# Kernel optimization log

Measured on AMD Instinct MI355X. Metric: run time of the kernel, lower is better.

Reference implementation:

```python
import jax, jax.numpy as jnp
import numpy as np

N, E, D = 50000, 800000, 256

def setup_inputs() -> dict:
    key = jax.random.key(0)
    ks = jax.random.split(key, 12)
    s = 1.0 / np.sqrt(D)
    return {
        "x": jax.random.normal(ks[0], (N, D), dtype=jnp.float32),
        "src": jax.random.randint(ks[1], (E,), 0, N, dtype=jnp.int64),
        "dst": jax.random.randint(ks[2], (E,), 0, N, dtype=jnp.int64),
        "W_w": jax.random.normal(ks[3], (D, D), dtype=jnp.float32) * s,
        "W_b": jnp.zeros((D,), dtype=jnp.float32),
        "U_w": jax.random.normal(ks[4], (D, D), dtype=jnp.float32) * s,
        "U_b": jnp.zeros((D,), dtype=jnp.float32),
        "V_w": jax.random.normal(ks[5], (D, D), dtype=jnp.float32) * s,
        "V_b": jnp.zeros((D,), dtype=jnp.float32),
        "attn_l": jax.random.normal(ks[6], (D,), dtype=jnp.float32) * s,
        "attn_r": jax.random.normal(ks[7], (D,), dtype=jnp.float32) * s,
        "gamma": jnp.ones((D,), dtype=jnp.float32),
        "beta": jnp.zeros((D,), dtype=jnp.float32),
    }

def reference(x, src, dst, W_w, W_b, U_w, U_b, V_w, V_b, attn_l, attn_r, gamma, beta):
    # node transforms (dropout p=0 -> identity)
    Wh = x @ W_w + W_b            # [N, D]
    Uh = x @ U_w + U_b            # [N, D]
    Vh = x @ V_w + V_b            # [N, D]
    out_src = Wh * attn_l         # [N, D]
    out_dst = Wh * attn_r         # [N, D]
    # per-edge gate: sigma = sigmoid(out_src[u] + out_dst[v])  [E, D]
    sigma = jax.nn.sigmoid(out_src[src] + out_dst[dst])
    # aggregate to destination nodes
    sum_sigma_h = jax.ops.segment_sum(Vh[src] * sigma, dst, num_segments=N)
    sum_sigma = jax.ops.segment_sum(sigma, dst, num_segments=N)
    h = Uh + sum_sigma_h / (sum_sigma + 1e-6)
    # layer norm (eps=1e-6, affine)
    mu = jnp.mean(h, axis=-1, keepdims=True)
    var = jnp.mean((h - mu) ** 2, axis=-1, keepdims=True)
    h = (h - mu) / jnp.sqrt(var + 1e-6) * gamma + beta
    h = jax.nn.relu(h)
    return x + h  # residual
```

## Files before the change

kernel.cpp:

```cpp
#include <hip/hip_runtime.h>
#include <hip/hip_bf16.h>

#define NN 50000
#define NE 800000
#define NB 196
#define NROWPAD 50048

#define XCVT_BLOCKS 6250
#define TW_BLOCKS   192
#define HIST_BLOCKS 3125

typedef __attribute__((ext_vector_type(8))) short short8;
typedef __attribute__((ext_vector_type(4))) float floatx4;
typedef unsigned short u16;
typedef unsigned int u32;

__device__ __forceinline__ u16 f2bf(float f) {
    u32 u = __float_as_uint(f);
    u += 0x7FFFu + ((u >> 16) & 1u);
    return (u16)(u >> 16);
}
__device__ __forceinline__ float bf_lo(u32 u) { return __uint_as_float(u << 16); }
__device__ __forceinline__ float bf_hi(u32 u) { return __uint_as_float(u & 0xFFFF0000u); }
__device__ __forceinline__ u32 pack_bf(float lo, float hi) {
    return (u32)f2bf(lo) | ((u32)f2bf(hi) << 16);
}
__device__ __forceinline__ void gl_lds16(const void* g, void* l) {
    __builtin_amdgcn_global_load_lds((const __attribute__((address_space(1))) void*)g,
                                     (__attribute__((address_space(3))) void*)l, 16, 0, 0);
}

#if __has_builtin(__builtin_amdgcn_exp2f)
#define EXP2F(x) __builtin_amdgcn_exp2f(x)
#else
#define EXP2F(x) exp2f(x)
#endif

__global__ __launch_bounds__(256) void prep_kernel(
    const float* __restrict__ x, u16* __restrict__ xbf,
    const float* __restrict__ W, const float* __restrict__ U, const float* __restrict__ V,
    u16* __restrict__ wT, const int* __restrict__ dst, int* __restrict__ deg, int do_xcvt) {
    __shared__ float s[32][33];
    int b = blockIdx.x;
    int xb = do_xcvt ? XCVT_BLOCKS : 0;
    if (b < xb) {
        size_t i = ((size_t)b * 256 + threadIdx.x) * 8;
        floatx4 f0 = *(const floatx4*)(x + i);
        floatx4 f1 = *(const floatx4*)(x + i + 4);
        uint4 pk;
        pk.x = pack_bf(f0[0], f0[1]);
        pk.y = pack_bf(f0[2], f0[3]);
        pk.z = pack_bf(f1[0], f1[1]);
        pk.w = pack_bf(f1[2], f1[3]);
        *(uint4*)(xbf + i) = pk;
    } else if (b < xb + TW_BLOCKS) {
        int bb = b - xb;
        int g = bb >> 6, rem = bb & 63;
        int r0 = (rem & 7) * 32, c0 = (rem >> 3) * 32;
        const float* M = (g == 0) ? W : ((g == 1) ? U : V);
        int tx = threadIdx.x & 31, ty = threadIdx.x >> 5;
#pragma unroll
        for (int k = 0; k < 4; ++k)
            s[ty + k * 8][tx] = M[(size_t)(r0 + ty + k * 8) * 256 + c0 + tx];
        __syncthreads();
#pragma unroll
        for (int k = 0; k < 4; ++k)
            wT[(size_t)(g * 256 + c0 + ty + k * 8) * 256 + r0 + tx] = f2bf(s[tx][ty + k * 8]);
    } else {
        int e = (b - xb - TW_BLOCKS) * 256 + threadIdx.x;
        if (e < NE) atomicAdd(&deg[dst[e]], 1);
    }
}

__global__ __launch_bounds__(256) void scanA_kernel(const int* __restrict__ deg, int* __restrict__ bsum) {
    int t = threadIdx.x;
    int i = blockIdx.x * 256 + t;
    int v = (i < NN) ? deg[i] : 0;
#pragma unroll
    for (int m = 32; m; m >>= 1) v += __shfl_xor(v, m, 64);
    __shared__ int ws[4];
    if ((t & 63) == 0) ws[t >> 6] = v;
    __syncthreads();
    if (t == 0) bsum[blockIdx.x] = ws[0] + ws[1] + ws[2] + ws[3];
}

__global__ __launch_bounds__(256) void scanB_kernel(const int* __restrict__ bsum, int* __restrict__ bpre,
                                                    int* __restrict__ rows_end) {
    int t = threadIdx.x, lane = t & 63, wv = t >> 6;
    int v = (t < NB) ? bsum[t] : 0;
    int inc = v;
#pragma unroll
    for (int off = 1; off < 64; off <<= 1) {
        int u = __shfl_up(inc, off, 64);
        if (lane >= off) inc += u;
    }
    __shared__ int wsum[4];
    if (lane == 63) wsum[wv] = inc;
    __syncthreads();
    int woff = 0;
    for (int k = 0; k < wv; ++k) woff += wsum[k];
    if (t < NB) bpre[t] = woff + inc - v;
    if (t == 255) rows_end[0] = woff + inc;
}

__global__ __launch_bounds__(256) void scanC_kernel(const int* __restrict__ deg, const int* __restrict__ bpre,
                                                    int* __restrict__ rows, int* __restrict__ cursor) {
    int t = threadIdx.x, lane = t & 63, wv = t >> 6;
    int i = blockIdx.x * 256 + t;
    int v = (i < NN) ? deg[i] : 0;
    int inc = v;
#pragma unroll
    for (int off = 1; off < 64; off <<= 1) {
        int u = __shfl_up(inc, off, 64);
        if (lane >= off) inc += u;
    }
    __shared__ int wsum[4];
    if (lane == 63) wsum[wv] = inc;
    __syncthreads();
    int woff = bpre[blockIdx.x];
    for (int k = 0; k < wv; ++k) woff += wsum[k];
    int excl = woff + inc - v;
    if (i < NN) { rows[i] = excl; cursor[i] = excl; }
}

__global__ void scatter_kernel(const int* __restrict__ src, const int* __restrict__ dst,
                               int* __restrict__ cursor, int* __restrict__ esrc) {
    int e = blockIdx.x * 256 + threadIdx.x;
    if (e < NE) {
        int d = dst[e];
        int pos = atomicAdd(&cursor[d], 1);
        esrc[pos] = src[e];
    }
}

template<bool USE_BF>
__global__ __launch_bounds__(256, 2) void gemm2_kernel(
    const u16* __restrict__ xbf, const float* __restrict__ xf, const u16* __restrict__ wT,
    const float* __restrict__ Wb, const float* __restrict__ Ub, const float* __restrict__ Vb,
    u16* __restrict__ WVh, float* __restrict__ Uh) {
    __shared__ __align__(16) u16 Bs[128 * 256];

    int rb = blockIdx.x * 128;
    int cgy = blockIdx.y;
    int cbg = cgy * 128;
    int t = threadIdx.x, lane = t & 63, w = t >> 6;

    int arow = rb + w * 32 + (lane & 15);
    short8 afr[2][8];
    if (USE_BF) {
#pragma unroll
        for (int rg = 0; rg < 2; ++rg)
#pragma unroll
            for (int ks = 0; ks < 8; ++ks)
                afr[rg][ks] = *(const short8*)(xbf + (size_t)(arow + rg * 16) * 256 + ks * 32 + (lane >> 4) * 8);
    } else {
#pragma unroll
        for (int rg = 0; rg < 2; ++rg)
#pragma unroll
            for (int ks = 0; ks < 8; ++ks) {
                int row = arow + rg * 16;
                const float* p = xf + ((size_t)(row < NN ? row : 0)) * 256 + ks * 32 + (lane >> 4) * 8;
                floatx4 f0 = *(const floatx4*)(p);
                floatx4 f1 = *(const floatx4*)(p + 4);
                uint4 pk;
                pk.x = pack_bf(f0[0], f0[1]);
                pk.y = pack_bf(f0[2], f0[3]);
                pk.z = pack_bf(f1[0], f1[1]);
                pk.w = pack_bf(f1[2], f1[3]);
                afr[rg][ks] = *(short8*)&pk;
            }
    }

#pragma unroll
    for (int i = 0; i < 16; ++i) {
        int ci = (w * 16 + i) * 2 + (lane >> 5);
        int q = (lane & 31) ^ (ci & 7);
        gl_lds16(wT + (size_t)(cbg + ci) * 256 + q * 8, Bs + (w * 16 + i) * 512);
    }
    __syncthreads();

    floatx4 acc[2][8] = {};
#pragma unroll
    for (int ks = 0; ks < 8; ++ks) {
#pragma unroll
        for (int cf = 0; cf < 8; ++cf) {
            int ci = cf * 16 + (lane & 15);
            int q = (ks * 4 + (lane >> 4)) ^ (ci & 7);
            short8 bfrag = *(const short8*)(Bs + ci * 256 + q * 8);
            acc[0][cf] = __builtin_amdgcn_mfma_f32_16x16x32_bf16(afr[0][ks], bfrag, acc[0][cf], 0, 0, 0);
            acc[1][cf] = __builtin_amdgcn_mfma_f32_16x16x32_bf16(afr[1][ks], bfrag, acc[1][cf], 0, 0, 0);
        }
    }

    int g = cbg >> 8;
    int cloc = cbg & 255;
    const float* bias = (g == 0) ? Wb : ((g == 1) ? Ub : Vb);
#pragma unroll
    for (int rg = 0; rg < 2; ++rg)
#pragma unroll
        for (int cf = 0; cf < 8; ++cf) {
            int col = cloc + cf * 16 + (lane & 15);
            float bv = bias[col];
#pragma unroll
            for (int r = 0; r < 4; ++r) {
                int row = rb + w * 32 + rg * 16 + (lane >> 4) * 4 + r;
                if (row < NN) {
                    float val = acc[rg][cf][r] + bv;
                    if (g == 0)      WVh[(size_t)row * 512 + col] = f2bf(val);
                    else if (g == 1) Uh[(size_t)row * 256 + col] = val;
                    else             WVh[(size_t)row * 512 + 256 + col] = f2bf(val);
                }
            }
        }
}

__global__ __launch_bounds__(256) void node_kernel(
    const u16* __restrict__ WVh, const float* __restrict__ x,
    const int* __restrict__ rows, const int* __restrict__ esrc,
    const float* __restrict__ attn_l, const float* __restrict__ attn_r,
    const float* __restrict__ gamma, const float* __restrict__ beta,
    float* inout) {
    int wv = threadIdx.x >> 6, lane = threadIdx.x & 63;
    int v = blockIdx.x * 4 + wv;
    if (v >= NN) return;
    int c0 = lane * 4;

    const float NL2E = -1.44269504f;
    floatx4 alv = *(const floatx4*)(attn_l + c0);
    floatx4 arv = *(const floatx4*)(attn_r + c0);
    uint2 wvv = *(const uint2*)(WVh + (size_t)v * 512 + c0);
    float al2[4] = { alv[0] * NL2E, alv[1] * NL2E, alv[2] * NL2E, alv[3] * NL2E };
    float td2[4] = { bf_lo(wvv.x) * arv[0] * NL2E, bf_hi(wvv.x) * arv[1] * NL2E,
                     bf_lo(wvv.y) * arv[2] * NL2E, bf_hi(wvv.y) * arv[3] * NL2E };

    float acc_h[4] = {0.f, 0.f, 0.f, 0.f};
    float acc_s[4] = {0.f, 0.f, 0.f, 0.f};

    auto edge = [&](uint2 wu, uint2 vu) {
        float wf[4] = { bf_lo(wu.x), bf_hi(wu.x), bf_lo(wu.y), bf_hi(wu.y) };
        float vf[4] = { bf_lo(vu.x), bf_hi(vu.x), bf_lo(vu.y), bf_hi(vu.y) };
#pragma unroll
        for (int j = 0; j < 4; ++j) {
            float m = fmaf(wf[j], al2[j], td2[j]);
            float s = __builtin_amdgcn_rcpf(1.0f + EXP2F(m));
            acc_s[j] += s;
            acc_h[j] = fmaf(s, vf[j], acc_h[j]);
        }
    };

    int e = rows[v], e1 = rows[v + 1];
    for (; e + 8 <= e1; e += 8) {
        int us[8];
#pragma unroll
        for (int q = 0; q < 8; ++q) us[q] = esrc[e + q];
        uint2 wu[8], vu[8];
#pragma unroll
        for (int q = 0; q < 8; ++q) {
            const u16* p = WVh + (size_t)us[q] * 512 + c0;
            wu[q] = *(const uint2*)p;
            vu[q] = *(const uint2*)(p + 256);
        }
#pragma unroll
        for (int q = 0; q < 8; ++q) edge(wu[q], vu[q]);
    }
    for (; e + 2 <= e1; e += 2) {
        int ua = esrc[e], ub = esrc[e + 1];
        const u16* pa = WVh + (size_t)ua * 512 + c0;
        const u16* pb = WVh + (size_t)ub * 512 + c0;
        uint2 wa = *(const uint2*)pa, va = *(const uint2*)(pa + 256);
        uint2 wb = *(const uint2*)pb, vb = *(const uint2*)(pb + 256);
        edge(wa, va); edge(wb, vb);
    }
    for (; e < e1; ++e) {
        int u = esrc[e];
        const u16* p = WVh + (size_t)u * 512 + c0;
        uint2 wu = *(const uint2*)p, vu = *(const uint2*)(p + 256);
        edge(wu, vu);
    }

    floatx4 uh = *(const floatx4*)(inout + (size_t)v * 256 + c0);
    float h[4];
#pragma unroll
    for (int j = 0; j < 4; ++j)
        h[j] = uh[j] + acc_h[j] * __builtin_amdgcn_rcpf(acc_s[j] + 1e-6f);

    float s01 = h[0] + h[1] + h[2] + h[3];
#pragma unroll
    for (int m = 32; m; m >>= 1) s01 += __shfl_xor(s01, m, 64);
    float mu = s01 * (1.0f / 256.0f);
    float d[4] = { h[0] - mu, h[1] - mu, h[2] - mu, h[3] - mu };
    float sq = d[0] * d[0] + d[1] * d[1] + d[2] * d[2] + d[3] * d[3];
#pragma unroll
    for (int m = 32; m; m >>= 1) sq += __shfl_xor(sq, m, 64);
    float inv = rsqrtf(sq * (1.0f / 256.0f) + 1e-6f);

    floatx4 gm = *(const floatx4*)(gamma + c0);
    floatx4 bt = *(const floatx4*)(beta + c0);
    floatx4 xr = *(const floatx4*)(x + (size_t)v * 256 + c0);
    floatx4 res;
#pragma unroll
    for (int j = 0; j < 4; ++j) {
        float y = d[j] * inv * gm[j] + bt[j];
        y = fmaxf(y, 0.0f);
        res[j] = xr[j] + y;
    }
    *(floatx4*)(inout + (size_t)v * 256 + c0) = res;
}

extern "C" void kernel_launch(void* const* d_in, const int* in_sizes, int n_in,
                              void* d_out, int out_size, void* d_ws, size_t ws_size,
                              hipStream_t stream) {
    const float* x       = (const float*)d_in[0];
    const int*   src     = (const int*)d_in[1];
    const int*   dst     = (const int*)d_in[2];
    const float* W_w     = (const float*)d_in[3];
    const float* W_b     = (const float*)d_in[4];
    const float* U_w     = (const float*)d_in[5];
    const float* U_b     = (const float*)d_in[6];
    const float* V_w     = (const float*)d_in[7];
    const float* V_b     = (const float*)d_in[8];
    const float* attn_l  = (const float*)d_in[9];
    const float* attn_r  = (const float*)d_in[10];
    const float* gamma   = (const float*)d_in[11];
    const float* beta    = (const float*)d_in[12];

    char* ws = (char*)d_ws;
    size_t off = 0;
    auto alloc = [&](size_t bytes) -> char* {
        char* p = ws + off;
        off += (bytes + 255) & ~(size_t)255;
        return p;
    };
    u16* WVh     = (u16*)alloc((size_t)NN * 512 * 2);
    u16* wT      = (u16*)alloc((size_t)768 * 256 * 2);
    int* deg     = (int*)alloc((size_t)NN * 4);
    int* rows    = (int*)alloc((size_t)(NN + 1) * 4);
    int* cursor  = (int*)alloc((size_t)NN * 4);
    int* esrc    = (int*)alloc((size_t)NE * 4);
    int* bsum    = (int*)alloc((size_t)NB * 4);
    int* bpre    = (int*)alloc((size_t)NB * 4);
    u16* xbf     = (u16*)alloc((size_t)NROWPAD * 256 * 2);
    bool use_bf  = (ws_size >= off);

    float* Uh_f32 = (float*)d_out;

    hipMemsetAsync(deg, 0, (size_t)NN * 4, stream);

    int xb = use_bf ? XCVT_BLOCKS : 0;
    prep_kernel<<<xb + TW_BLOCKS + HIST_BLOCKS, 256, 0, stream>>>(
        x, xbf, W_w, U_w, V_w, wT, dst, deg, use_bf ? 1 : 0);

    scanA_kernel<<<NB, 256, 0, stream>>>(deg, bsum);
    scanB_kernel<<<1, 256, 0, stream>>>(bsum, bpre, rows + NN);
    scanC_kernel<<<NB, 256, 0, stream>>>(deg, bpre, rows, cursor);
    scatter_kernel<<<(NE + 255) / 256, 256, 0, stream>>>(src, dst, cursor, esrc);

    dim3 gg((NN + 127) / 128, 6);
    if (use_bf) {
        gemm2_kernel<true><<<gg, 256, 0, stream>>>(xbf, x, wT, W_b, U_b, V_b, WVh, Uh_f32);
    } else {
        gemm2_kernel<false><<<gg, 256, 0, stream>>>(nullptr, x, wT, W_b, U_b, V_b, WVh, Uh_f32);
    }

    node_kernel<<<(NN + 3) / 4, 256, 0, stream>>>(
        WVh, x, rows, esrc, attn_l, attn_r, gamma, beta, (float*)d_out);
}
```

Measured before the change: 304.7 us.

## Store Wh in FP8, read B from global, remap GEMM blocks per XCD

The Wh projection used for the edge gates is now stored in FP8, cutting the per-edge gather of Wh in the node kernel from 8 to 4 bytes per lane. The GEMM drops its LDS staging of the weight tile and loads B fragments straight from global memory. Operands are swapped so each lane writes contiguous vectorised outputs, and workgroups are remapped so neighbouring tiles land on the same XCD. FP8 rounding of Wh adds precision error to the sigmoid gate inputs.

```diff
diff --git a/kernel.cpp b/kernel.cpp
--- a/kernel.cpp
+++ b/kernel.cpp
@@ -9,9 +9,19 @@
 #define XCVT_BLOCKS 6250
 #define TW_BLOCKS   192
 #define HIST_BLOCKS 3125
+#define GEMM_NWG    2346
+
+#if __has_builtin(__builtin_amdgcn_cvt_pk_fp8_f32) && __has_builtin(__builtin_amdgcn_cvt_pk_f32_fp8)
+#define HAVE_FP8 1
+#define ROWB 768
+#else
+#define HAVE_FP8 0
+#define ROWB 1024
+#endif
 
 typedef __attribute__((ext_vector_type(8))) short short8;
 typedef __attribute__((ext_vector_type(4))) float floatx4;
+typedef __attribute__((ext_vector_type(2))) float floatx2;
 typedef unsigned short u16;
 typedef unsigned int u32;
 
@@ -24,10 +34,6 @@
 __device__ __forceinline__ float bf_hi(u32 u) { return __uint_as_float(u & 0xFFFF0000u); }
 __device__ __forceinline__ u32 pack_bf(float lo, float hi) {
     return (u32)f2bf(lo) | ((u32)f2bf(hi) << 16);
-}
-__device__ __forceinline__ void gl_lds16(const void* g, void* l) {
-    __builtin_amdgcn_global_load_lds((const __attribute__((address_space(1))) void*)g,
-                                     (__attribute__((address_space(3))) void*)l, 16, 0, 0);
 }
 
 #if __has_builtin(__builtin_amdgcn_exp2f)
@@ -134,15 +140,17 @@
 }
 
 template<bool USE_BF>
-__global__ __launch_bounds__(256, 2) void gemm2_kernel(
+__global__ __launch_bounds__(256, 2) void gemm3_kernel(
     const u16* __restrict__ xbf, const float* __restrict__ xf, const u16* __restrict__ wT,
     const float* __restrict__ Wb, const float* __restrict__ Ub, const float* __restrict__ Vb,
-    u16* __restrict__ WVh, float* __restrict__ Uh) {
-    __shared__ __align__(16) u16 Bs[128 * 256];
-
-    int rb = blockIdx.x * 128;
-    int cgy = blockIdx.y;
+    char* __restrict__ WVh, float* __restrict__ Uh) {
+    int orig = blockIdx.x;
+    int xcd = orig & 7, j = orig >> 3;
+    int wgid = (xcd < 2 ? xcd * 294 : 2 * 294 + (xcd - 2) * 293) + j;
+    int rb = (wgid / 6) * 128;
+    int cgy = wgid % 6;
     int cbg = cgy * 128;
+
     int t = threadIdx.x, lane = t & 63, w = t >> 6;
 
     int arow = rb + w * 32 + (lane & 15);
@@ -171,51 +179,62 @@
             }
     }
 
-#pragma unroll
-    for (int i = 0; i < 16; ++i) {
-        int ci = (w * 16 + i) * 2 + (lane >> 5);
-        int q = (lane & 31) ^ (ci & 7);
-        gl_lds16(wT + (size_t)(cbg + ci) * 256 + q * 8, Bs + (w * 16 + i) * 512);
-    }
-    __syncthreads();
-
+    const u16* wTb = wT + (size_t)(cbg + (lane & 15)) * 256 + (lane >> 4) * 8;
     floatx4 acc[2][8] = {};
 #pragma unroll
     for (int ks = 0; ks < 8; ++ks) {
 #pragma unroll
         for (int cf = 0; cf < 8; ++cf) {
-            int ci = cf * 16 + (lane & 15);
-            int q = (ks * 4 + (lane >> 4)) ^ (ci & 7);
-            short8 bfrag = *(const short8*)(Bs + ci * 256 + q * 8);
-            acc[0][cf] = __builtin_amdgcn_mfma_f32_16x16x32_bf16(afr[0][ks], bfrag, acc[0][cf], 0, 0, 0);
-            acc[1][cf] = __builtin_amdgcn_mfma_f32_16x16x32_bf16(afr[1][ks], bfrag, acc[1][cf], 0, 0, 0);
-        }
-    }
-
-    int g = cbg >> 8;
-    int cloc = cbg & 255;
+            short8 bfrag = *(const short8*)(wTb + (size_t)cf * 16 * 256 + ks * 32);
+            acc[0][cf] = __builtin_amdgcn_mfma_f32_16x16x32_bf16(bfrag, afr[0][ks], acc[0][cf], 0, 0, 0);
+            acc[1][cf] = __builtin_amdgcn_mfma_f32_16x16x32_bf16(bfrag, afr[1][ks], acc[1][cf], 0, 0, 0);
+        }
+    }
+
+    int g = cgy >> 1;
+    int cloc = (cgy & 1) * 128;
     const float* bias = (g == 0) ? Wb : ((g == 1) ? Ub : Vb);
-#pragma unroll
-    for (int rg = 0; rg < 2; ++rg)
+
+#pragma unroll
+    for (int rg = 0; rg < 2; ++rg) {
+        int noderow = rb + w * 32 + rg * 16 + (lane & 15);
+        if (noderow >= NN) continue;
 #pragma unroll
         for (int cf = 0; cf < 8; ++cf) {
-            int col = cloc + cf * 16 + (lane & 15);
-            float bv = bias[col];
-#pragma unroll
-            for (int r = 0; r < 4; ++r) {
-                int row = rb + w * 32 + rg * 16 + (lane >> 4) * 4 + r;
-                if (row < NN) {
-                    float val = acc[rg][cf][r] + bv;
-                    if (g == 0)      WVh[(size_t)row * 512 + col] = f2bf(val);
-                    else if (g == 1) Uh[(size_t)row * 256 + col] = val;
-                    else             WVh[(size_t)row * 512 + 256 + col] = f2bf(val);
-                }
+            int colc = cloc + cf * 16 + (lane >> 4) * 4;
+            floatx4 bv = *(const floatx4*)(bias + colc);
+            float v0 = acc[rg][cf][0] + bv[0];
+            float v1 = acc[rg][cf][1] + bv[1];
+            float v2 = acc[rg][cf][2] + bv[2];
+            float v3 = acc[rg][cf][3] + bv[3];
+            if (g == 1) {
+                floatx4 o = { v0, v1, v2, v3 };
+                *(floatx4*)(Uh + (size_t)noderow * 256 + colc) = o;
+            } else if (g == 0) {
+#if HAVE_FP8
+                u32 p = 0;
+                p = __builtin_amdgcn_cvt_pk_fp8_f32(v0, v1, p, false);
+                p = __builtin_amdgcn_cvt_pk_fp8_f32(v2, v3, p, true);
+                *(u32*)(WVh + (size_t)noderow * ROWB + colc) = p;
+#else
+                uint2 o = { pack_bf(v0, v1), pack_bf(v2, v3) };
+                *(uint2*)(WVh + (size_t)noderow * ROWB + colc * 2) = o;
+#endif
+            } else {
+#if HAVE_FP8
+                uint2 o = { pack_bf(v0, v1), pack_bf(v2, v3) };
+                *(uint2*)(WVh + (size_t)noderow * ROWB + 256 + colc * 2) = o;
+#else
+                uint2 o = { pack_bf(v0, v1), pack_bf(v2, v3) };
+                *(uint2*)(WVh + (size_t)noderow * ROWB + 512 + colc * 2) = o;
+#endif
             }
         }
+    }
 }
 
 __global__ __launch_bounds__(256) void node_kernel(
-    const u16* __restrict__ WVh, const float* __restrict__ x,
+    const char* __restrict__ WVh, const float* __restrict__ x,
     const int* __restrict__ rows, const int* __restrict__ esrc,
     const float* __restrict__ attn_l, const float* __restrict__ attn_r,
     const float* __restrict__ gamma, const float* __restrict__ beta,
@@ -228,16 +247,34 @@
     const float NL2E = -1.44269504f;
     floatx4 alv = *(const floatx4*)(attn_l + c0);
     floatx4 arv = *(const floatx4*)(attn_r + c0);
-    uint2 wvv = *(const uint2*)(WVh + (size_t)v * 512 + c0);
+
+    float mywf[4];
+#if HAVE_FP8
+    {
+        u32 myw = *(const u32*)(WVh + (size_t)v * ROWB + lane * 4);
+        floatx2 a = __builtin_amdgcn_cvt_pk_f32_fp8(myw, false);
+        floatx2 b = __builtin_amdgcn_cvt_pk_f32_fp8(myw, true);
+        mywf[0] = a[0]; mywf[1] = a[1]; mywf[2] = b[0]; mywf[3] = b[1];
+    }
+#else
+    {
+        uint2 myw = *(const uint2*)(WVh + (size_t)v * ROWB + lane * 8);
+        mywf[0] = bf_lo(myw.x); mywf[1] = bf_hi(myw.x);
+        mywf[2] = bf_lo(myw.y); mywf[3] = bf_hi(myw.y);
+    }
+#endif
     float al2[4] = { alv[0] * NL2E, alv[1] * NL2E, alv[2] * NL2E, alv[3] * NL2E };
-    float td2[4] = { bf_lo(wvv.x) * arv[0] * NL2E, bf_hi(wvv.x) * arv[1] * NL2E,
-                     bf_lo(wvv.y) * arv[2] * NL2E, bf_hi(wvv.y) * arv[3] * NL2E };
+    float td2[4] = { mywf[0] * arv[0] * NL2E, mywf[1] * arv[1] * NL2E,
+                     mywf[2] * arv[2] * NL2E, mywf[3] * arv[3] * NL2E };
 
     float acc_h[4] = {0.f, 0.f, 0.f, 0.f};
     float acc_s[4] = {0.f, 0.f, 0.f, 0.f};
 
-    auto edge = [&](uint2 wu, uint2 vu) {
-        float wf[4] = { bf_lo(wu.x), bf_hi(wu.x), bf_lo(wu.y), bf_hi(wu.y) };
+#if HAVE_FP8
+    auto edge = [&](u32 w8, uint2 vu) {
+        floatx2 a = __builtin_amdgcn_cvt_pk_f32_fp8(w8, false);
+        floatx2 b = __builtin_amdgcn_cvt_pk_f32_fp8(w8, true);
+        float wf[4] = { a[0], a[1], b[0], b[1] };
         float vf[4] = { bf_lo(vu.x), bf_hi(vu.x), bf_lo(vu.y), bf_hi(vu.y) };
 #pragma unroll
         for (int j = 0; j < 4; ++j) {
@@ -247,36 +284,57 @@
             acc_h[j] = fmaf(s, vf[j], acc_h[j]);
         }
     };
-
     int e = rows[v], e1 = rows[v + 1];
     for (; e + 8 <= e1; e += 8) {
         int us[8];
 #pragma unroll
         for (int q = 0; q < 8; ++q) us[q] = esrc[e + q];
+        u32 w8[8]; uint2 vu[8];
+#pragma unroll
+        for (int q = 0; q < 8; ++q) {
+            const char* p = WVh + (size_t)us[q] * ROWB;
+            w8[q] = *(const u32*)(p + lane * 4);
+            vu[q] = *(const uint2*)(p + 256 + lane * 8);
+        }
+#pragma unroll
+        for (int q = 0; q < 8; ++q) edge(w8[q], vu[q]);
+    }
+    for (; e < e1; ++e) {
+        const char* p = WVh + (size_t)esrc[e] * ROWB;
+        edge(*(const u32*)(p + lane * 4), *(const uint2*)(p + 256 + lane * 8));
+    }
+#else
+    auto edge = [&](uint2 wu, uint2 vu) {
+        float wf[4] = { bf_lo(wu.x), bf_hi(wu.x), bf_lo(wu.y), bf_hi(wu.y) };
+        float vf[4] = { bf_lo(vu.x), bf_hi(vu.x), bf_lo(vu.y), bf_hi(vu.y) };
+#pragma unroll
+        for (int j = 0; j < 4; ++j) {
+            float m = fmaf(wf[j], al2[j], td2[j]);
+            float s = __builtin_amdgcn_rcpf(1.0f + EXP2F(m));
+            acc_s[j] += s;
+            acc_h[j] = fmaf(s, vf[j], acc_h[j]);
+        }
+    };
+    int e = rows[v], e1 = rows[v + 1];
+    for (; e + 8 <= e1; e += 8) {
+        int us[8];
+#pragma unroll
+        for (int q = 0; q < 8; ++q) us[q] = esrc[e + q];
         uint2 wu[8], vu[8];
 #pragma unroll
         for (int q = 0; q < 8; ++q) {
-            const u16* p = WVh + (size_t)us[q] * 512 + c0;
-            wu[q] = *(const uint2*)p;
-            vu[q] = *(const uint2*)(p + 256);
+            const char* p = WVh + (size_t)us[q] * ROWB;
+            wu[q] = *(const uint2*)(p + lane * 8);
+            vu[q] = *(const uint2*)(p + 512 + lane * 8);
         }
 #pragma unroll
         for (int q = 0; q < 8; ++q) edge(wu[q], vu[q]);
     }
-    for (; e + 2 <= e1; e += 2) {
-        int ua = esrc[e], ub = esrc[e + 1];
-        const u16* pa = WVh + (size_t)ua * 512 + c0;
-        const u16* pb = WVh + (size_t)ub * 512 + c0;
-        uint2 wa = *(const uint2*)pa, va = *(const uint2*)(pa + 256);
-        uint2 wb = *(const uint2*)pb, vb = *(const uint2*)(pb + 256);
-        edge(wa, va); edge(wb, vb);
-    }
     for (; e < e1; ++e) {
-        int u = esrc[e];
-        const u16* p = WVh + (size_t)u * 512 + c0;
-        uint2 wu = *(const uint2*)p, vu = *(const uint2*)(p + 256);
-        edge(wu, vu);
-    }
+        const char* p = WVh + (size_t)esrc[e] * ROWB;
+        edge(*(const uint2*)(p + lane * 8), *(const uint2*)(p + 512 + lane * 8));
+    }
+#endif
 
     floatx4 uh = *(const floatx4*)(inout + (size_t)v * 256 + c0);
     float h[4];
@@ -331,7 +389,7 @@
         off += (bytes + 255) & ~(size_t)255;
         return p;
     };
-    u16* WVh     = (u16*)alloc((size_t)NN * 512 * 2);
+    char* WVh    = alloc((size_t)NN * ROWB);
     u16* wT      = (u16*)alloc((size_t)768 * 256 * 2);
     int* deg     = (int*)alloc((size_t)NN * 4);
     int* rows    = (int*)alloc((size_t)(NN + 1) * 4);
@@ -355,11 +413,10 @@
     scanC_kernel<<<NB, 256, 0, stream>>>(deg, bpre, rows, cursor);
     scatter_kernel<<<(NE + 255) / 256, 256, 0, stream>>>(src, dst, cursor, esrc);
 
-    dim3 gg((NN + 127) / 128, 6);
     if (use_bf) {
-        gemm2_kernel<true><<<gg, 256, 0, stream>>>(xbf, x, wT, W_b, U_b, V_b, WVh, Uh_f32);
+        gemm3_kernel<true><<<GEMM_NWG, 256, 0, stream>>>(xbf, x, wT, W_b, U_b, V_b, WVh, Uh_f32);
     } else {
-        gemm2_kernel<false><<<gg, 256, 0, stream>>>(nullptr, x, wT, W_b, U_b, V_b, WVh, Uh_f32);
+        gemm3_kernel<false><<<GEMM_NWG, 256, 0, stream>>>(nullptr, x, wT, W_b, U_b, V_b, WVh, Uh_f32);
     }
 
     node_kernel<<<(NN + 3) / 4, 256, 0, stream>>>(
```

After: 316.3 us. +3.8%, slower.
